# Optimization experiments

Measured on AMD Instinct MI355X. Metric: run time of the kernel, lower is better.

Reference implementation:

```python
import jax, jax.numpy as jnp
import numpy as np

IN_CH = 64
OUT_CH = 32
SCALE = 2
BLOCK = SCALE ** 3  # 8
N = 400000   # input sparse voxels (lines in pair_fwd)
M = 200000   # output sparse voxels


def setup_inputs() -> dict:
    key = jax.random.key(0)
    k1, k2, k3 = jax.random.split(key, 3)
    x_features = jax.random.normal(k1, (N, IN_CH), dtype=jnp.float32)
    # flat ParameterList: weights[i*BLOCK + j] is the (in_channels,) weight for
    # output channel i, kernel position j
    weights = jax.random.normal(k2, (BLOCK * OUT_CH, IN_CH), dtype=jnp.float32)
    # spconv pair_fwd: [kernel_volume, num_lines], -1 marks invalid mapping
    pair_fwd = jax.random.randint(k3, (BLOCK, N), -1, M)
    return {"x_features": x_features, "weights": weights,
            "pair_fwd": pair_fwd, "num_out": M}


def reference(x_features, weights, pair_fwd, num_out):
    block, n = pair_fwd.shape
    out_ch = weights.shape[0] // block
    # W[o, j, c] == weights_list[o*block + j]
    W = weights.reshape(out_ch, block, -1)
    # sequential VoxelShuffle then .view(-1) per block is identity on each
    # voxel's in_channels feature vector, so:
    # vals[j, n, o] = dot(W[o, j, :], x_features[n, :])
    vals = jnp.einsum('nc,ojc->jno', x_features, W)  # [block, N, out_ch]
    idx = pair_fwd.reshape(-1)                       # [block*N]
    # route invalid (-1) entries to a dummy trailing row
    safe = jnp.where(idx >= 0, idx, num_out)
    buf = jnp.zeros((num_out + 1, out_ch), dtype=vals.dtype)
    # original uses assignment (set) semantics into out_features
    buf = buf.at[safe].set(vals.reshape(block * n, out_ch))
    return buf[:num_out]
```

## Files before the change

### kernel.cpp

```cpp
#include <hip/hip_runtime.h>

#define IN_CH  64
#define OUT_CH 32
#define BLOCK  8
#define ROWS   8


__device__ __forceinline__ float bflo(unsigned u) { return __uint_as_float(u << 16); }
__device__ __forceinline__ float bfhi(unsigned u) { return __uint_as_float(u & 0xffff0000u); }

__global__ void k_fill_m1(int4* __restrict__ p, int n4) {
    int i = blockIdx.x * 256 + threadIdx.x;
    if (i < n4) p[i] = make_int4(-1, -1, -1, -1);
}

__global__ void k_transpose_bf16(const float* __restrict__ w, unsigned* __restrict__ wt) {
    int d = blockIdx.x * 256 + threadIdx.x;
    if (d >= BLOCK * OUT_CH * IN_CH / 2) return;
    int q  = d & 3;
    int o  = (d >> 2) & 31;
    int j  = (d >> 7) & 7;
    int c8 = d >> 10;
    int c  = c8 * 8 + q * 2;
    float f0 = w[(o * BLOCK + j) * IN_CH + c];
    float f1 = w[(o * BLOCK + j) * IN_CH + c + 1];
    auto cvt = [](float f) -> unsigned {
        unsigned u = __float_as_uint(f);
        return (u + 0x7fffu + ((u >> 16) & 1u)) >> 16;
    };
    wt[d] = cvt(f0) | (cvt(f1) << 16);
}

__global__ void k_scatter_range(const int* __restrict__ pair, int* __restrict__ argmax,
                                int N, int jhi, int jlo, int flip) {
    int n = blockIdx.x * 256 + threadIdx.x;
    if (n >= N) return;
    if (flip) n = N - 1 - n;
    for (int j = jhi; j >= jlo; --j) {
        int t = j * N + n;
        int m = pair[t];
        if (m >= 0 && argmax[m] < t)
            atomicMax(&argmax[m], t);
    }
}

__global__ __launch_bounds__(512, 4) void k_compute(
        const float* __restrict__ x, const uint4* __restrict__ wt,
        const int* __restrict__ argmax, float* __restrict__ out, int M, int N) {
    __shared__ uint4 Wl[2048];
    __shared__ __align__(16) float Xl[8][2][ROWS * 64];
    for (int i = threadIdx.x; i < 2048; i += 512) Wl[i] = wt[i];
    __syncthreads();

    const int lane = threadIdx.x & 63;
    const int o    = lane & 31;
    const int h    = lane >> 5;
    const int wv   = threadIdx.x >> 6;
    const unsigned uN = (unsigned)N;

    int gw   = blockIdx.x * 8 + wv;
    int base = gw * 64;
    if (base >= M) return;
    int nrows = min(64, M - base);

    int t0 = ((base + lane) < M) ? argmax[base + lane] : -1;
    int jn = 8, nn = 0;
    if (t0 >= 0) {
        unsigned j = (unsigned)t0 / uN;
        nn = t0 - (int)(j * uN);
        jn = (int)j;
    }

    int ntiles = (nrows + ROWS - 1) / ROWS;
    float ld[ROWS];

#pragma unroll
    for (int r = 0; r < ROWS; ++r) {
        int n = __shfl(nn, r);
        ld[r] = x[(size_t)n * IN_CH + lane];
    }

    for (int tile = 0; tile < ntiles; ++tile) {
        float* buf = &Xl[wv][tile & 1][0];
#pragma unroll
        for (int r = 0; r < ROWS; ++r)
            buf[r * 64 + lane] = ld[r];

        if (tile + 1 < ntiles) {
            int nb = (tile + 1) * ROWS;
#pragma unroll
            for (int r = 0; r < ROWS; ++r) {
                int n = __shfl(nn, nb + r);
                ld[r] = x[(size_t)n * IN_CH + lane];
            }
        }

        asm volatile("s_waitcnt lgkmcnt(0)" ::: "memory");

#pragma unroll 2
        for (int r = 0; r < ROWS; ++r) {
            int grow = tile * ROWS + r;
            int jc   = __shfl(jn, grow);
            const float4* xp = (const float4*)(buf + r * 64) + h * 8;
            const uint4*  wp = Wl + h * 1024 + (jc & 7) * 32 + o;
            float ax = 0.f, ay = 0.f, az = 0.f, aw = 0.f;
#pragma unroll
            for (int k = 0; k < 4; ++k) {
                uint4  wq  = wp[k * 256];
                float4 xv0 = xp[k * 2];
                float4 xv1 = xp[k * 2 + 1];
                ax = fmaf(bflo(wq.x), xv0.x, ax);
                ay = fmaf(bfhi(wq.x), xv0.y, ay);
                az = fmaf(bflo(wq.y), xv0.z, az);
                aw = fmaf(bfhi(wq.y), xv0.w, aw);
                ax = fmaf(bflo(wq.z), xv1.x, ax);
                ay = fmaf(bfhi(wq.z), xv1.y, ay);
                az = fmaf(bflo(wq.w), xv1.z, az);
                aw = fmaf(bfhi(wq.w), xv1.w, aw);
            }
            float s = (ax + ay) + (az + aw);
            s += __shfl_xor(s, 32);
            if (jc == 8) s = 0.f;
            if (h == 0 && grow < nrows)
                out[(size_t)(base + grow) * OUT_CH + o] = s;
        }
    }
}

extern "C" void kernel_launch(void* const* d_in, const int* in_sizes, int n_in,
                              void* d_out, int out_size, void* d_ws, size_t ws_size,
                              hipStream_t stream) {
    const float* x    = (const float*)d_in[0];
    const float* w    = (const float*)d_in[1];
    const int*   pair = (const int*)d_in[2];
    int N = in_sizes[0] / IN_CH;
    int M = out_size / OUT_CH;

    char*     ws     = (char*)d_ws;
    int*      argmax = (int*)ws;
    unsigned* wt     = (unsigned*)(ws + (size_t)M * 4);

    int n4 = M / 4;
    k_fill_m1<<<(n4 + 255) / 256, 256, 0, stream>>>((int4*)argmax, n4);

    int gN = (N + 255) / 256;
    k_transpose_bf16<<<(BLOCK * OUT_CH * IN_CH / 2 + 255) / 256, 256, 0, stream>>>(w, wt);
    k_scatter_range<<<gN, 256, 0, stream>>>(pair, argmax, N, 7, 7, 1);
    k_scatter_range<<<gN, 256, 0, stream>>>(pair, argmax, N, 6, 6, 0);
    k_scatter_range<<<gN, 256, 0, stream>>>(pair, argmax, N, 5, 0, 0);

    int waves  = (M + 63) / 64;
    int blocks = (waves + 7) / 8;
    k_compute<<<blocks, 512, 0, stream>>>(x, (const uint4*)wt, argmax,
                                          (float*)d_out, M, N);
}
```

Before: 100.5 us.

## Merge prep kernels, collapse scatter passes, use readlane and pair-row stores

Fuses the argmax fill and weight bf16 transpose into one kernel and merges the second and third scatter passes into one, cutting launch count. In the compute kernel, per-row indices are read with scalar readlane instead of shuffles, and the j indices for each tile are fetched up front. Two rows are processed per step so both wave halves write output, which halves the store instructions. Fewer scatter passes may raise atomic contention, and the prep kernel relies on the grid covering the weight range (M/4 threads far exceeds 8192).

New measurement: 96.34 us. 1.04x faster.

```diff
diff --git a/kernel.cpp b/kernel.cpp
--- a/kernel.cpp
+++ b/kernel.cpp
@@ -9,26 +9,24 @@
 __device__ __forceinline__ float bflo(unsigned u) { return __uint_as_float(u << 16); }
 __device__ __forceinline__ float bfhi(unsigned u) { return __uint_as_float(u & 0xffff0000u); }
 
-__global__ void k_fill_m1(int4* __restrict__ p, int n4) {
+__global__ void k_prep(const float* __restrict__ w, unsigned* __restrict__ wt,
+                       int4* __restrict__ argmax4, int n4) {
     int i = blockIdx.x * 256 + threadIdx.x;
-    if (i < n4) p[i] = make_int4(-1, -1, -1, -1);
-}
-
-__global__ void k_transpose_bf16(const float* __restrict__ w, unsigned* __restrict__ wt) {
-    int d = blockIdx.x * 256 + threadIdx.x;
-    if (d >= BLOCK * OUT_CH * IN_CH / 2) return;
-    int q  = d & 3;
-    int o  = (d >> 2) & 31;
-    int j  = (d >> 7) & 7;
-    int c8 = d >> 10;
-    int c  = c8 * 8 + q * 2;
-    float f0 = w[(o * BLOCK + j) * IN_CH + c];
-    float f1 = w[(o * BLOCK + j) * IN_CH + c + 1];
-    auto cvt = [](float f) -> unsigned {
-        unsigned u = __float_as_uint(f);
-        return (u + 0x7fffu + ((u >> 16) & 1u)) >> 16;
-    };
-    wt[d] = cvt(f0) | (cvt(f1) << 16);
+    if (i < n4) argmax4[i] = make_int4(-1, -1, -1, -1);
+    if (i < BLOCK * OUT_CH * IN_CH / 2) {
+        int q  = i & 3;
+        int o  = (i >> 2) & 31;
+        int j  = (i >> 7) & 7;
+        int c8 = i >> 10;
+        int c  = c8 * 8 + q * 2;
+        float f0 = w[(o * BLOCK + j) * IN_CH + c];
+        float f1 = w[(o * BLOCK + j) * IN_CH + c + 1];
+        auto cvt = [](float f) -> unsigned {
+            unsigned u = __float_as_uint(f);
+            return (u + 0x7fffu + ((u >> 16) & 1u)) >> 16;
+        };
+        wt[i] = cvt(f0) | (cvt(f1) << 16);
+    }
 }
 
 __global__ void k_scatter_range(const int* __restrict__ pair, int* __restrict__ argmax,
@@ -42,6 +40,30 @@
         if (m >= 0 && argmax[m] < t)
             atomicMax(&argmax[m], t);
     }
+}
+
+__device__ __forceinline__ float row_dot(const float* __restrict__ buf, int r, int jcv,
+                                         const uint4* __restrict__ Wl, int o, int h) {
+    const float4* xp = (const float4*)(buf + r * 64) + h * 8;
+    const uint4*  wp = Wl + h * 1024 + (jcv & 7) * 32 + o;
+    float ax = 0.f, ay = 0.f, az = 0.f, aw = 0.f;
+#pragma unroll
+    for (int k = 0; k < 4; ++k) {
+        uint4  wq  = wp[k * 256];
+        float4 xv0 = xp[k * 2];
+        float4 xv1 = xp[k * 2 + 1];
+        ax = fmaf(bflo(wq.x), xv0.x, ax);
+        ay = fmaf(bfhi(wq.x), xv0.y, ay);
+        az = fmaf(bflo(wq.y), xv0.z, az);
+        aw = fmaf(bfhi(wq.y), xv0.w, aw);
+        ax = fmaf(bflo(wq.z), xv1.x, ax);
+        ay = fmaf(bfhi(wq.z), xv1.y, ay);
+        az = fmaf(bflo(wq.w), xv1.z, az);
+        aw = fmaf(bfhi(wq.w), xv1.w, aw);
+    }
+    float s = (ax + ay) + (az + aw);
+    s += __shfl_xor(s, 32);
+    return (jcv == 8) ? 0.f : s;
 }
 
 __global__ __launch_bounds__(512, 4) void k_compute(
@@ -76,12 +98,18 @@
 
 #pragma unroll
     for (int r = 0; r < ROWS; ++r) {
-        int n = __shfl(nn, r);
+        int n = __builtin_amdgcn_readlane(nn, r);
         ld[r] = x[(size_t)n * IN_CH + lane];
     }
 
     for (int tile = 0; tile < ntiles; ++tile) {
         float* buf = &Xl[wv][tile & 1][0];
+
+        int jc[ROWS];
+#pragma unroll
+        for (int r = 0; r < ROWS; ++r)
+            jc[r] = __builtin_amdgcn_readlane(jn, tile * ROWS + r);
+
 #pragma unroll
         for (int r = 0; r < ROWS; ++r)
             buf[r * 64 + lane] = ld[r];
@@ -90,39 +118,22 @@
             int nb = (tile + 1) * ROWS;
 #pragma unroll
             for (int r = 0; r < ROWS; ++r) {
-                int n = __shfl(nn, nb + r);
+                int n = __builtin_amdgcn_readlane(nn, nb + r);
                 ld[r] = x[(size_t)n * IN_CH + lane];
             }
         }
 
         asm volatile("s_waitcnt lgkmcnt(0)" ::: "memory");
 
-#pragma unroll 2
-        for (int r = 0; r < ROWS; ++r) {
+#pragma unroll
+        for (int r = 0; r < ROWS; r += 2) {
             int grow = tile * ROWS + r;
-            int jc   = __shfl(jn, grow);
-            const float4* xp = (const float4*)(buf + r * 64) + h * 8;
-            const uint4*  wp = Wl + h * 1024 + (jc & 7) * 32 + o;
-            float ax = 0.f, ay = 0.f, az = 0.f, aw = 0.f;
-#pragma unroll
-            for (int k = 0; k < 4; ++k) {
-                uint4  wq  = wp[k * 256];
-                float4 xv0 = xp[k * 2];
-                float4 xv1 = xp[k * 2 + 1];
-                ax = fmaf(bflo(wq.x), xv0.x, ax);
-                ay = fmaf(bfhi(wq.x), xv0.y, ay);
-                az = fmaf(bflo(wq.y), xv0.z, az);
-                aw = fmaf(bfhi(wq.y), xv0.w, aw);
-                ax = fmaf(bflo(wq.z), xv1.x, ax);
-                ay = fmaf(bfhi(wq.z), xv1.y, ay);
-                az = fmaf(bflo(wq.w), xv1.z, az);
-                aw = fmaf(bfhi(wq.w), xv1.w, aw);
-            }
-            float s = (ax + ay) + (az + aw);
-            s += __shfl_xor(s, 32);
-            if (jc == 8) s = 0.f;
-            if (h == 0 && grow < nrows)
-                out[(size_t)(base + grow) * OUT_CH + o] = s;
+            float s0 = row_dot(buf, r,     jc[r],     Wl, o, h);
+            float s1 = row_dot(buf, r + 1, jc[r + 1], Wl, o, h);
+            float sv   = h ? s1 : s0;
+            int   orow = grow + h;
+            if (orow < nrows)
+                out[(size_t)(base + orow) * OUT_CH + o] = sv;
         }
     }
 }
@@ -141,13 +152,11 @@
     unsigned* wt     = (unsigned*)(ws + (size_t)M * 4);
 
     int n4 = M / 4;
-    k_fill_m1<<<(n4 + 255) / 256, 256, 0, stream>>>((int4*)argmax, n4);
+    k_prep<<<(n4 + 255) / 256, 256, 0, stream>>>(w, wt, (int4*)argmax, n4);
 
     int gN = (N + 255) / 256;
-    k_transpose_bf16<<<(BLOCK * OUT_CH * IN_CH / 2 + 255) / 256, 256, 0, stream>>>(w, wt);
     k_scatter_range<<<gN, 256, 0, stream>>>(pair, argmax, N, 7, 7, 1);
-    k_scatter_range<<<gN, 256, 0, stream>>>(pair, argmax, N, 6, 6, 0);
-    k_scatter_range<<<gN, 256, 0, stream>>>(pair, argmax, N, 5, 0, 0);
+    k_scatter_range<<<gN, 256, 0, stream>>>(pair, argmax, N, 6, 0, 0);
 
     int waves  = (M + 63) / 64;
     int blocks = (waves + 7) / 8;
```
